# Performance work log

Measured on AMD Instinct MI355X. Metric: run time of the kernel, lower is better.

## Reference

```python
import jax, jax.numpy as jnp
import numpy as np


def pool_windows(a, k):
    # a: [..., H, W] with k == stride (non-overlapping windows)
    lead = a.shape[:-2]
    H, W = a.shape[-2], a.shape[-1]
    a = a.reshape(*lead, H // k, k, W // k, k)
    a = jnp.moveaxis(a, -3, -2)            # [..., Ho, Wo, k, k]
    return a.reshape(*lead, H // k, W // k, k * k)


def setup_inputs() -> dict:
    key = jax.random.key(0)
    k1, k2 = jax.random.split(key)
    S, C, H, W = 258, 64, 64, 64
    x = jax.random.normal(k1, (S, C, H, W), dtype=jnp.float32)
    # noise layer (last row) is nonnegative by convention
    x = x.at[-1].set(jnp.abs(x[-1]))
    x_true = jax.random.normal(k2, (C, H, W), dtype=jnp.float32)
    return {"x": x, "x_true": x_true, "kernel_size": 2, "stride": 2}


def reference(x, x_true, kernel_size, stride):
    # Zonotope/interval abstract transformer for MaxPool2d.
    # x: [S, C, H, W]; row 0 = center, rows 1:-1 = eps coeffs, row -1 = noise.
    assert kernel_size == stride
    k = kernel_size

    # Interval bounds per element (sum-of-abs reduction over symbol layers)
    eps_abs = jnp.sum(jnp.abs(x[1:]), axis=0)           # [C, H, W]
    lo = x[0] - eps_abs
    hi = x[0] + eps_abs

    xw = pool_windows(x, k)                              # [S, C, Ho, Wo, K]
    lw = pool_windows(lo, k)                             # [C, Ho, Wo, K]
    uw = pool_windows(hi, k)
    K = xw.shape[-1]

    # Candidate: window element with the largest lower bound
    i_star = jnp.argmax(lw, axis=-1)                     # [C, Ho, Wo]
    l_star = jnp.take_along_axis(lw, i_star[..., None], axis=-1)[..., 0]
    u_max = jnp.max(uw, axis=-1)

    # Max upper bound among the other window elements
    oh = jnp.arange(K) == i_star[..., None]              # one-hot of i_star
    u_other = jnp.max(jnp.where(oh, -jnp.inf, uw), axis=-1)

    # Exact case: the candidate dominates every other element -> pass its
    # affine form through. Otherwise fall back to the sound interval box
    # [l_star, u_max] (center +/- half-width in the noise layer).
    exact = l_star >= u_other                            # [C, Ho, Wo]

    gathered = jnp.take_along_axis(
        xw, i_star[None, ..., None], axis=-1)[..., 0]    # [S, C, Ho, Wo]

    box_center = 0.5 * (l_star + u_max)
    box_noise = 0.5 * (u_max - l_star)

    out_center = jnp.where(exact, gathered[0], box_center)
    out_eps = jnp.where(exact[None], gathered[1:-1], 0.0)
    out_noise = jnp.where(exact, jnp.abs(gathered[-1]), box_noise)

    x_out = jnp.concatenate(
        [out_center[None], out_eps, out_noise[None]], axis=0)

    out_abs = jnp.sum(jnp.abs(x_out[1:]), axis=0)
    x_min = x_out[0] - out_abs
    x_max = x_out[0] + out_abs

    x_true_out = jnp.max(pool_windows(x_true, k), axis=-1)
    return x_out, x_min, x_max, x_true_out
```

## Files before the change

### kernel.cpp

```cpp
#include <hip/hip_runtime.h>
#include <math.h>

#define S    258
#define C    64
#define H    64
#define W    64
#define HO   32
#define WO   32
#define NP   (C * HO * WO)
#define L    (C * H * W)
#define XOUT (S * NP)

__global__ __launch_bounds__(256) void k_fused(const float* __restrict__ x,
                                               const float* __restrict__ x_true,
                                               float* __restrict__ out) {
    __shared__ float red[16][8][16];
    __shared__ float eps2[8][16];
    __shared__ int   ex_p[32];
    __shared__ int   ex_pos[32];
    __shared__ int   ex_n;

    const int b   = blockIdx.x;
    const int c   = b >> 5;
    const int ho  = b & 31;
    const int tid = threadIdx.x;
    const int sg  = tid >> 4;
    const int wp  = tid & 15;

    if (tid == 0) ex_n = 0;

    const int p0      = b * 32;
    const int rowbase = c * (H * W) + ho * 2 * W;

    #pragma unroll 4
    for (int i = tid; i < 256 * 32; i += 256) {
        const int s = 1 + (i >> 5);
        out[(size_t)s * NP + p0 + (i & 31)] = 0.0f;
    }

    const int s0 = 1 + ((257 * sg) >> 4);
    const int s1 = 1 + ((257 * (sg + 1)) >> 4);
    const int A  = rowbase + wp * 4;

    float a0=0.f,a1=0.f,a2=0.f,a3=0.f,a4=0.f,a5=0.f,a6=0.f,a7=0.f;
    const float* px = x + (size_t)s0 * L + A;
    for (int s = s0; s < s1; ++s) {
        float4 t = *(const float4*)(px);
        float4 u = *(const float4*)(px + W);
        a0 += fabsf(t.x); a1 += fabsf(t.y); a2 += fabsf(t.z); a3 += fabsf(t.w);
        a4 += fabsf(u.x); a5 += fabsf(u.y); a6 += fabsf(u.z); a7 += fabsf(u.w);
        px += L;
    }
    red[sg][0][wp]=a0; red[sg][1][wp]=a1; red[sg][2][wp]=a2; red[sg][3][wp]=a3;
    red[sg][4][wp]=a4; red[sg][5][wp]=a5; red[sg][6][wp]=a6; red[sg][7][wp]=a7;
    __syncthreads();

    if (tid < 128) {
        const int e = tid >> 4, w = tid & 15;
        float sum = 0.f;
        #pragma unroll
        for (int j = 0; j < 16; ++j) sum += red[j][e][w];
        eps2[e][w] = sum;
    }
    __syncthreads();

    if (tid < 32) {
        const int wo  = tid;
        const int wq  = wo >> 1;
        const int odd = wo & 1;
        float eps[4];
        eps[0] = eps2[odd * 2 + 0][wq];
        eps[1] = eps2[odd * 2 + 1][wq];
        eps[2] = eps2[4 + odd * 2 + 0][wq];
        eps[3] = eps2[4 + odd * 2 + 1][wq];

        const int wbase = rowbase + wo * 2;
        float2 r0 = *(const float2*)(x + wbase);
        float2 r1 = *(const float2*)(x + wbase + W);
        float x0[4] = { r0.x, r0.y, r1.x, r1.y };
        float lo[4], hi[4];
        #pragma unroll
        for (int e = 0; e < 4; ++e) { lo[e] = x0[e] - eps[e]; hi[e] = x0[e] + eps[e]; }

        int istar = 0;
        #pragma unroll
        for (int e = 1; e < 4; ++e) if (lo[e] > lo[istar]) istar = e;

        const float lstar = lo[istar];
        const float umax  = fmaxf(fmaxf(hi[0], hi[1]), fmaxf(hi[2], hi[3]));
        float uoth = -INFINITY;
        #pragma unroll
        for (int e = 0; e < 4; ++e) if (e != istar) uoth = fmaxf(uoth, hi[e]);

        const bool exact = (lstar >= uoth);
        const int  pos   = wbase + (istar & 1) + (istar >> 1) * W;

        float center, noise;
        if (exact) {
            center = x0[istar];
            noise  = fabsf(x[(size_t)(S - 1) * L + pos]);
            int i  = atomicAdd(&ex_n, 1);
            ex_p[i]   = p0 + wo;
            ex_pos[i] = pos;
        } else {
            center = 0.5f * (lstar + umax);
            noise  = 0.5f * (umax - lstar);
        }

        const int p = p0 + wo;
        out[p] = center;
        out[(size_t)(S - 1) * NP + p] = noise;
        out[XOUT + p] = lstar;
        out[XOUT + NP + p] = umax;

        float2 t0 = *(const float2*)(x_true + wbase);
        float2 t1 = *(const float2*)(x_true + wbase + W);
        out[XOUT + 2 * NP + p] = fmaxf(fmaxf(t0.x, t0.y), fmaxf(t1.x, t1.y));
    }
    __syncthreads();

    const int n = ex_n;
    for (int j = 0; j < n; ++j) {
        const int s = 1 + tid;
        out[(size_t)s * NP + ex_p[j]] = x[(size_t)s * L + ex_pos[j]];
    }
}

extern "C" void kernel_launch(void* const* d_in, const int* in_sizes, int n_in,
                              void* d_out, int out_size, void* d_ws, size_t ws_size,
                              hipStream_t stream) {
    const float* x      = (const float*)d_in[0];
    const float* x_true = (const float*)d_in[1];
    float* out = (float*)d_out;
    k_fused<<<C * HO, 256, 0, stream>>>(x, x_true, out);
}
```

Measured before the change: 386.2 us.

## Split fused pooling kernel into partial-sum reduction and decision kernels

Replaces the single fused kernel with two launches. The first spreads the sum-of-abs reduction over 8 symbol chunks, 64 channels and 4 quarter-planes (2048 blocks), writing partial sums to workspace with coalesced float4 loads, and also zeroes the eps output rows. The second sums the 8 partials per element, makes the exact-vs-box decision with all 256 threads active, and gathers eps rows for exact windows. This aims to fix low per-thread work and the old layout where only 32 of 256 threads did the decision, in exchange for an extra launch and a workspace round trip.

```diff
diff --git a/kernel.cpp b/kernel.cpp
--- a/kernel.cpp
+++ b/kernel.cpp
@@ -5,124 +5,121 @@
 #define C    64
 #define H    64
 #define W    64
-#define HO   32
-#define WO   32
-#define NP   (C * HO * WO)
-#define L    (C * H * W)
+#define NP   65536
+#define L    262144
 #define XOUT (S * NP)
+#define NSC  8
+#define NQ   4
 
-__global__ __launch_bounds__(256) void k_fused(const float* __restrict__ x,
-                                               const float* __restrict__ x_true,
-                                               float* __restrict__ out) {
-    __shared__ float red[16][8][16];
-    __shared__ float eps2[8][16];
-    __shared__ int   ex_p[32];
-    __shared__ int   ex_pos[32];
-    __shared__ int   ex_n;
+__global__ __launch_bounds__(256) void k_partial(const float* __restrict__ x,
+                                                 float* __restrict__ part,
+                                                 float* __restrict__ out) {
+    const int b  = blockIdx.x;
+    const int sc = b >> 8;
+    const int c  = (b >> 2) & 63;
+    const int q  = b & 3;
+    const int t  = threadIdx.x;
 
-    const int b   = blockIdx.x;
-    const int c   = b >> 5;
-    const int ho  = b & 31;
-    const int tid = threadIdx.x;
-    const int sg  = tid >> 4;
-    const int wp  = tid & 15;
-
-    if (tid == 0) ex_n = 0;
-
-    const int p0      = b * 32;
-    const int rowbase = c * (H * W) + ho * 2 * W;
-
-    #pragma unroll 4
-    for (int i = tid; i < 256 * 32; i += 256) {
-        const int s = 1 + (i >> 5);
-        out[(size_t)s * NP + p0 + (i & 31)] = 0.0f;
+    {
+        float4 z = make_float4(0.f, 0.f, 0.f, 0.f);
+        float4* zp = (float4*)(out + NP) + (size_t)b * 2048 + t;
+        #pragma unroll
+        for (int i = 0; i < 8; ++i) zp[i * 256] = z;
     }
 
-    const int s0 = 1 + ((257 * sg) >> 4);
-    const int s1 = 1 + ((257 * (sg + 1)) >> 4);
-    const int A  = rowbase + wp * 4;
+    const int s0 = 1 + ((257 * sc) >> 3);
+    const int s1 = 1 + ((257 * (sc + 1)) >> 3);
 
-    float a0=0.f,a1=0.f,a2=0.f,a3=0.f,a4=0.f,a5=0.f,a6=0.f,a7=0.f;
-    const float* px = x + (size_t)s0 * L + A;
+    const int base = c * (H * W) + q * 1024 + 4 * t;
+    const float* px = x + (size_t)s0 * L + base;
+    float4 acc = make_float4(0.f, 0.f, 0.f, 0.f);
+    #pragma unroll 4
     for (int s = s0; s < s1; ++s) {
-        float4 t = *(const float4*)(px);
-        float4 u = *(const float4*)(px + W);
-        a0 += fabsf(t.x); a1 += fabsf(t.y); a2 += fabsf(t.z); a3 += fabsf(t.w);
-        a4 += fabsf(u.x); a5 += fabsf(u.y); a6 += fabsf(u.z); a7 += fabsf(u.w);
+        float4 v = *(const float4*)px;
+        acc.x += fabsf(v.x); acc.y += fabsf(v.y);
+        acc.z += fabsf(v.z); acc.w += fabsf(v.w);
         px += L;
     }
-    red[sg][0][wp]=a0; red[sg][1][wp]=a1; red[sg][2][wp]=a2; red[sg][3][wp]=a3;
-    red[sg][4][wp]=a4; red[sg][5][wp]=a5; red[sg][6][wp]=a6; red[sg][7][wp]=a7;
+    *(float4*)(part + (size_t)sc * L + c * (H * W) + q * 1024 + 4 * t) = acc;
+}
+
+__global__ __launch_bounds__(256) void k_decide(const float* __restrict__ x,
+                                                const float* __restrict__ x_true,
+                                                const float* __restrict__ part,
+                                                float* __restrict__ out) {
+    __shared__ int ex_n;
+    __shared__ int ex_p[256];
+    __shared__ int ex_pos[256];
+
+    const int b = blockIdx.x;
+    const int c = b >> 2;
+    const int q = b & 3;
+    const int t = threadIdx.x;
+    if (t == 0) ex_n = 0;
     __syncthreads();
 
-    if (tid < 128) {
-        const int e = tid >> 4, w = tid & 15;
-        float sum = 0.f;
-        #pragma unroll
-        for (int j = 0; j < 16; ++j) sum += red[j][e][w];
-        eps2[e][w] = sum;
+    const int r  = t >> 5;
+    const int wo = t & 31;
+    const int qbase   = c * (H * W) + q * 1024;
+    const int loc_top = (2 * r) * W + 2 * wo;
+    const int loc_bot = loc_top + W;
+
+    float e0 = 0.f, e1 = 0.f, e2 = 0.f, e3 = 0.f;
+    #pragma unroll
+    for (int sc = 0; sc < NSC; ++sc) {
+        const float* pp = part + (size_t)sc * L + qbase;
+        float2 a = *(const float2*)(pp + loc_top);
+        float2 d = *(const float2*)(pp + loc_bot);
+        e0 += a.x; e1 += a.y; e2 += d.x; e3 += d.y;
     }
+
+    float2 r0 = *(const float2*)(x + qbase + loc_top);
+    float2 r1 = *(const float2*)(x + qbase + loc_bot);
+    float x0[4]  = { r0.x, r0.y, r1.x, r1.y };
+    float eps[4] = { e0, e1, e2, e3 };
+    float lo[4], hi[4];
+    #pragma unroll
+    for (int e = 0; e < 4; ++e) { lo[e] = x0[e] - eps[e]; hi[e] = x0[e] + eps[e]; }
+
+    int istar = 0;
+    #pragma unroll
+    for (int e = 1; e < 4; ++e) if (lo[e] > lo[istar]) istar = e;
+
+    const float lstar = lo[istar];
+    const float umax  = fmaxf(fmaxf(hi[0], hi[1]), fmaxf(hi[2], hi[3]));
+    float uoth = -INFINITY;
+    #pragma unroll
+    for (int e = 0; e < 4; ++e) if (e != istar) uoth = fmaxf(uoth, hi[e]);
+
+    const bool exact = (lstar >= uoth);
+    const int  pos   = qbase + loc_top + (istar & 1) + (istar >> 1) * W;
+
+    float center, noise;
+    if (exact) {
+        center = x0[istar];
+        noise  = fabsf(x[(size_t)(S - 1) * L + pos]);
+        int i  = atomicAdd(&ex_n, 1);
+        ex_p[i]   = c * 1024 + q * 256 + t;
+        ex_pos[i] = pos;
+    } else {
+        center = 0.5f * (lstar + umax);
+        noise  = 0.5f * (umax - lstar);
+    }
+
+    const int p = c * 1024 + q * 256 + t;
+    out[p] = center;
+    out[(size_t)(S - 1) * NP + p] = noise;
+    out[XOUT + p] = lstar;
+    out[XOUT + NP + p] = umax;
+
+    float2 t0 = *(const float2*)(x_true + qbase + loc_top);
+    float2 t1 = *(const float2*)(x_true + qbase + loc_bot);
+    out[XOUT + 2 * NP + p] = fmaxf(fmaxf(t0.x, t0.y), fmaxf(t1.x, t1.y));
+
     __syncthreads();
-
-    if (tid < 32) {
-        const int wo  = tid;
-        const int wq  = wo >> 1;
-        const int odd = wo & 1;
-        float eps[4];
-        eps[0] = eps2[odd * 2 + 0][wq];
-        eps[1] = eps2[odd * 2 + 1][wq];
-        eps[2] = eps2[4 + odd * 2 + 0][wq];
-        eps[3] = eps2[4 + odd * 2 + 1][wq];
-
-        const int wbase = rowbase + wo * 2;
-        float2 r0 = *(const float2*)(x + wbase);
-        float2 r1 = *(const float2*)(x + wbase + W);
-        float x0[4] = { r0.x, r0.y, r1.x, r1.y };
-        float lo[4], hi[4];
-        #pragma unroll
-        for (int e = 0; e < 4; ++e) { lo[e] = x0[e] - eps[e]; hi[e] = x0[e] + eps[e]; }
-
-        int istar = 0;
-        #pragma unroll
-        for (int e = 1; e < 4; ++e) if (lo[e] > lo[istar]) istar = e;
-
-        const float lstar = lo[istar];
-        const float umax  = fmaxf(fmaxf(hi[0], hi[1]), fmaxf(hi[2], hi[3]));
-        float uoth = -INFINITY;
-        #pragma unroll
-        for (int e = 0; e < 4; ++e) if (e != istar) uoth = fmaxf(uoth, hi[e]);
-
-        const bool exact = (lstar >= uoth);
-        const int  pos   = wbase + (istar & 1) + (istar >> 1) * W;
-
-        float center, noise;
-        if (exact) {
-            center = x0[istar];
-            noise  = fabsf(x[(size_t)(S - 1) * L + pos]);
-            int i  = atomicAdd(&ex_n, 1);
-            ex_p[i]   = p0 + wo;
-            ex_pos[i] = pos;
-        } else {
-            center = 0.5f * (lstar + umax);
-            noise  = 0.5f * (umax - lstar);
-        }
-
-        const int p = p0 + wo;
-        out[p] = center;
-        out[(size_t)(S - 1) * NP + p] = noise;
-        out[XOUT + p] = lstar;
-        out[XOUT + NP + p] = umax;
-
-        float2 t0 = *(const float2*)(x_true + wbase);
-        float2 t1 = *(const float2*)(x_true + wbase + W);
-        out[XOUT + 2 * NP + p] = fmaxf(fmaxf(t0.x, t0.y), fmaxf(t1.x, t1.y));
-    }
-    __syncthreads();
-
     const int n = ex_n;
     for (int j = 0; j < n; ++j) {
-        const int s = 1 + tid;
-        out[(size_t)s * NP + ex_p[j]] = x[(size_t)s * L + ex_pos[j]];
+        out[(size_t)(1 + t) * NP + ex_p[j]] = x[(size_t)(1 + t) * L + ex_pos[j]];
     }
 }
 
@@ -131,6 +128,9 @@
                               hipStream_t stream) {
     const float* x      = (const float*)d_in[0];
     const float* x_true = (const float*)d_in[1];
-    float* out = (float*)d_out;
-    k_fused<<<C * HO, 256, 0, stream>>>(x, x_true, out);
+    float* out  = (float*)d_out;
+    float* part = (float*)d_ws;
+
+    k_partial<<<NSC * C * NQ, 256, 0, stream>>>(x, part, out);
+    k_decide<<<C * NQ, 256, 0, stream>>>(x, x_true, part, out);
 }
```

New measurement: 384.4 us. No clear change (-0.5%).
